# Kernel optimization log

Measured on AMD Instinct MI355X. Metric: run time of the kernel, lower is better.

## Reference

```python
import jax, jax.numpy as jnp
from jax import lax
import numpy as np

N_BASIS = 256
N_FREQ = 128
N_TIME = 8
LAM = 0.2
LR = 1e-3
B1, B2, EPS = 0.9, 0.999, 1e-8
CONV_TOL = 1e-3


def setup_inputs() -> dict:
    key = jax.random.key(0)
    k1, k2 = jax.random.split(key)
    spec = jax.random.normal(k1, (32, N_FREQ, 256), dtype=jnp.float32)
    basis = jax.random.normal(k2, (N_FREQ * N_TIME, N_BASIS), dtype=jnp.float32)
    return {"spec": spec, "basis": basis, "n_iter_coef": 30, "pad": 0, "stride": 4}


def normalize01(x):
    # torch normalize01 with dims=-1, keepdims
    xmin = x.min(axis=-1, keepdims=True)
    xmax = x.max(axis=-1, keepdims=True)
    return (x - xmin) / (xmax - xmin)


def _response(x, basis, n_iter):
    # x: [B, D]; Adam-optimize coef [B, N_BASIS] for n_iter steps with the
    # same early-stop rule as the torch code (frozen via a done flag).
    B = x.shape[0]
    sig = jnp.std(x, ddof=1)  # torch .std() is unbiased over all elements

    def loss_fn(coef):
        pred = coef @ basis.T                      # [B, D]
        mse = jnp.mean((pred - x) ** 2)
        return mse + LAM * sig * jnp.mean(jnp.abs(coef / sig))

    coef0 = jnp.full((B, N_BASIS), 0.5 / N_BASIS, dtype=jnp.float32)
    m0 = jnp.zeros_like(coef0)
    v0 = jnp.zeros_like(coef0)

    def body(carry, _):
        coef, m, v, t, old_loss, done = carry
        loss, g = jax.value_and_grad(loss_fn)(coef)
        t_new = t + 1.0
        m_new = B1 * m + (1.0 - B1) * g
        v_new = B2 * v + (1.0 - B2) * g * g
        mhat = m_new / (1.0 - B1 ** t_new)
        vhat = v_new / (1.0 - B2 ** t_new)
        coef_new = coef - LR * mhat / (jnp.sqrt(vhat) + EPS)
        conv = jnp.abs(old_loss - loss) / old_loss < CONV_TOL
        sel = lambda a, b: jnp.where(done, a, b)
        new_carry = (
            sel(coef, coef_new),
            sel(m, m_new),
            sel(v, v_new),
            jnp.where(done, t, t_new),
            jnp.where(done, old_loss, loss),
            done | conv,
        )
        return new_carry, None

    init = (coef0, m0, v0, jnp.float32(0.0), jnp.float32(1e-10), jnp.array(False))
    (coef, _, _, _, _, _), _ = lax.scan(body, init, None, length=n_iter)
    return coef  # detached in torch


def reference(spec, basis, n_iter_coef, pad, stride):
    if spec.ndim == 2:
        spec = spec[None, ...]
    B, F, T = spec.shape
    spec_ = jnp.pad(spec, ((0, 0), (0, 0), (pad, pad)))
    starts = np.arange(0, T - N_TIME + 1, stride)          # window start frames
    idx = starts[:, None] + np.arange(N_TIME)              # [W, N_TIME]
    wins = spec_[:, :, idx]                                # [B, F, W, N_TIME]
    x = jnp.transpose(wins, (2, 0, 1, 3)).reshape(len(starts), B, F * N_TIME)
    x = normalize01(x)                                     # per row of [B, D]
    coef = jax.vmap(lambda xw: _response(xw, basis, n_iter_coef))(x)  # [W, B, N_BASIS]
    return jnp.transpose(coef, (1, 2, 0))                  # [B, N_BASIS, W]
```

## Files before the change

### kernel.cpp

```cpp
#include <hip/hip_runtime.h>
#include <math.h>

#define NB     256
#define NF     128
#define FT     1024
#define NW     63
#define TORIG  256
#define MAXIT  48
#define RPB    8
#define NBLK   4
#define GRID   256

typedef float f2 __attribute__((ext_vector_type(2)));
__device__ __forceinline__ f2 pkfma(f2 a, f2 b, f2 c) {
    return __builtin_elementwise_fma(a, b, c);
}

__device__ __forceinline__ float rl(float v, int lane) {
    return __uint_as_float((unsigned)__builtin_amdgcn_readlane((int)__float_as_uint(v), lane));
}

__device__ __forceinline__ int xidx(int k2, int cg, int row) {
    return (k2 * 512 + row * 64 + (cg ^ row)) * 4;
}

__global__ __launch_bounds__(512, 2) void window_kernel(
    const float* __restrict__ spec,
    const float* __restrict__ basis,
    float* __restrict__ G,
    const int* __restrict__ p_niter,
    const int* __restrict__ p_pad,
    const int* __restrict__ p_stride,
    double* __restrict__ sxbuf,
    double* __restrict__ gpart,
    unsigned int* __restrict__ gcnt,
    float* __restrict__ out)
{
    __shared__ float  s_p0[RPB * 2048];
    __shared__ float  s_p1[RPB * 2048];
    __shared__ float  s_gred[2][NB];
    __shared__ float  s_mn[RPB], s_rng[RPB];
    __shared__ double s_dred[8];
    __shared__ float  s_redq[2][8], s_redr[2][8];
    __shared__ unsigned int s_wcnt[2];
    __shared__ int    s_stop[2];
    float* const s_xn = s_p1;

    const int bid = blockIdx.x;
    const int yy  = bid >> 3;
    const int q   = yy & 3;
    const int w   = (bid & 7) + 8 * (yy >> 2);
    const int tid = threadIdx.x;
    const int ks  = tid >> 6;
    const int kg  = tid & 63;
    const int r   = kg >> 3;
    const int cgo = 8 * ks + (kg & 7);
    const int n_iter = p_niter[0];
    const int t0     = w * p_stride[0] - p_pad[0];
    unsigned int* gbar = gcnt + MAXIT * NW;

    {
        const int c = tid & 255, jh = tid >> 8;
        float acc = 0.f;
        const float* bp = basis + (size_t)(jh * 512) * NB;
        #pragma unroll 16
        for (int j = 0; j < 512; ++j)
            acc = fmaf(bp[j * NB + bid], bp[j * NB + c], acc);
        s_gred[jh][c] = acc;
        __syncthreads();
        if (jh == 0) G[(size_t)bid * NB + c] = s_gred[0][c] + s_gred[1][c];
    }
    __threadfence();
    __syncthreads();
    if (tid == 0) atomicAdd(gbar, 1u);
    if (w >= NW) return;

    #pragma unroll
    for (int i = 0; i < 16; ++i) {
        const int e = i * 512 + tid;
        const int b = e >> 10, jj = e & 1023;
        const int f = jj >> 3, t = jj & 7, tq = t0 + t;
        s_xn[b * FT + jj] = (tq >= 0 && tq < TORIG)
            ? spec[((size_t)(q * RPB + b) * NF + f) * TORIG + tq] : 0.f;
    }
    __syncthreads();
    {
        float mn = __builtin_inff(), mx = -__builtin_inff();
        #pragma unroll
        for (int i = 0; i < 16; ++i) {
            const float v = s_xn[ks * FT + i * 64 + kg];
            mn = fminf(mn, v); mx = fmaxf(mx, v);
        }
        #pragma unroll
        for (int off = 32; off; off >>= 1) {
            mn = fminf(mn, __shfl_down(mn, off));
            mx = fmaxf(mx, __shfl_down(mx, off));
        }
        if (kg == 0) { s_mn[ks] = mn; s_rng[ks] = mx - mn; }
    }
    __syncthreads();
    double sx2p = 0.0;
    #pragma unroll
    for (int i = 0; i < 16; ++i) {
        const int e = i * 512 + tid;
        const int b = e >> 10, jj = e & 1023;
        const float v = (s_xn[b * FT + jj] - s_mn[b]) / s_rng[b];
        s_xn[b * FT + jj] = v;
        sx2p += (double)v * (double)v;
    }
    #pragma unroll
    for (int off = 32; off; off >>= 1) sx2p += __shfl_down(sx2p, off);
    if (kg == 0) s_dred[ks] = sx2p;
    __syncthreads();
    if (tid == 0) {
        double s = 0.0;
        #pragma unroll
        for (int i = 0; i < 8; ++i) s += s_dred[i];
        sxbuf[w * NBLK + q] = s;
        __threadfence();
    }

    f2 xb01[RPB], xb23[RPB];
    #pragma unroll
    for (int b = 0; b < RPB; ++b) { xb01[b] = (f2){0.f, 0.f}; xb23[b] = (f2){0.f, 0.f}; }
    for (int i0 = 0; i0 < 128; i0 += 4) {
        const int jj = ks * 128 + i0;
        float4 bv[4];
        #pragma unroll
        for (int t = 0; t < 4; ++t)
            bv[t] = *(const float4*)(basis + (size_t)(jj + t) * NB + 4 * kg);
        #pragma unroll
        for (int b = 0; b < RPB; ++b) {
            const float4 x4 = *(const float4*)&s_xn[b * FT + jj];
            const f2 vx = {x4.x, x4.x}, vy = {x4.y, x4.y};
            const f2 vz = {x4.z, x4.z}, vw = {x4.w, x4.w};
            xb01[b] = pkfma(vx, (f2){bv[0].x, bv[0].y}, xb01[b]);
            xb23[b] = pkfma(vx, (f2){bv[0].z, bv[0].w}, xb23[b]);
            xb01[b] = pkfma(vy, (f2){bv[1].x, bv[1].y}, xb01[b]);
            xb23[b] = pkfma(vy, (f2){bv[1].z, bv[1].w}, xb23[b]);
            xb01[b] = pkfma(vz, (f2){bv[2].x, bv[2].y}, xb01[b]);
            xb23[b] = pkfma(vz, (f2){bv[2].z, bv[2].w}, xb23[b]);
            xb01[b] = pkfma(vw, (f2){bv[3].x, bv[3].y}, xb01[b]);
            xb23[b] = pkfma(vw, (f2){bv[3].z, bv[3].w}, xb23[b]);
        }
    }
    __syncthreads();
    #pragma unroll
    for (int b = 0; b < RPB; ++b)
        *(float4*)&s_p0[xidx(ks, kg, b)] =
            make_float4(xb01[b].x, xb01[b].y, xb23[b].x, xb23[b].y);
    __syncthreads();
    float xB[4] = {0.f, 0.f, 0.f, 0.f};
    #pragma unroll
    for (int k2 = 0; k2 < 8; ++k2) {
        const float4 p4 = *(const float4*)&s_p0[xidx(k2, cgo, r)];
        xB[0] += p4.x; xB[1] += p4.y; xB[2] += p4.z; xB[3] += p4.w;
    }

    if (tid == 0) {
        while (__hip_atomic_load(gbar, __ATOMIC_ACQUIRE, __HIP_MEMORY_SCOPE_AGENT) < (unsigned)GRID)
            __builtin_amdgcn_s_sleep(1);
    }
    if (tid == 64) { s_wcnt[0] = 0; s_wcnt[1] = 0; s_stop[0] = 0; s_stop[1] = 0; }
    __syncthreads();
    float4 g[32];
    #pragma unroll
    for (int kl = 0; kl < 32; ++kl)
        g[kl] = *(const float4*)(G + (size_t)(32 * ks + kl) * NB + 4 * kg);

    const float C0 = 0.5f / 256.f;
    float cf[4]  = {C0, C0, C0, C0}, cfp[4] = {C0, C0, C0, C0};
    float m_[4]  = {0, 0, 0, 0},    v_[4]  = {0, 0, 0, 0};
    float b1p = 1.f, b2p = 1.f;
    float old_loss = 1e-10f;
    double sxtot = 0.0;
    const float c1 = 2.f / 32768.f, c2 = 0.2f / 8192.f;
    int use_prev = 0;

    for (int it = 0; it < n_iter; ++it) {
        const int p = it & 1;
        float* const sp = p ? s_p1 : s_p0;

        if (tid == 64 && it >= 2) {
            const int itc = it - 2;
            while (__hip_atomic_load(&gcnt[itc * NW + w], __ATOMIC_ACQUIRE,
                                     __HIP_MEMORY_SCOPE_AGENT) < (unsigned)NBLK)
                __builtin_amdgcn_s_sleep(1);
            const size_t pbm = ((size_t)itc * NW + w) * NBLK;
            double Qt = 0.0, Rt = 0.0;
            #pragma unroll
            for (int i = 0; i < NBLK; ++i) {
                Qt += gpart[(pbm + i) * 2 + 0];
                Rt += gpart[(pbm + i) * 2 + 1];
            }
            if (itc == 0)
                sxtot = sxbuf[w * NBLK + 0] + sxbuf[w * NBLK + 1] +
                        sxbuf[w * NBLK + 2] + sxbuf[w * NBLK + 3];
            const float loss = (float)((Qt + sxtot) / 32768.0 + 0.2 * (Rt / 8192.0));
            const float stat = fabsf(old_loss - loss) / old_loss;
            old_loss = loss;
            s_stop[p] = (stat < 1e-3f) ? 1 : 0;
        }

        #pragma unroll
        for (int b = 0; b < RPB; ++b) {
            f2 a01 = {0.f, 0.f}, a23 = {0.f, 0.f};
            #pragma unroll
            for (int m = 0; m < 8; ++m) {
                const float4 ga = g[4 * m + 0], gb = g[4 * m + 1];
                const float4 gc = g[4 * m + 2], gd = g[4 * m + 3];
                const int L = b * 8 + m;
                const float sx = rl(cf[0], L), sy = rl(cf[1], L);
                const float sz = rl(cf[2], L), sw = rl(cf[3], L);
                const f2 vx = {sx, sx}, vy = {sy, sy}, vz = {sz, sz}, vw = {sw, sw};
                a01 = pkfma(vx, (f2){ga.x, ga.y}, a01);
                a23 = pkfma(vx, (f2){ga.z, ga.w}, a23);
                a01 = pkfma(vy, (f2){gb.x, gb.y}, a01);
                a23 = pkfma(vy, (f2){gb.z, gb.w}, a23);
                a01 = pkfma(vz, (f2){gc.x, gc.y}, a01);
                a23 = pkfma(vz, (f2){gc.z, gc.w}, a23);
                a01 = pkfma(vw, (f2){gd.x, gd.y}, a01);
                a23 = pkfma(vw, (f2){gd.z, gd.w}, a23);
            }
            *(float4*)&sp[xidx(ks, kg, b)] = make_float4(a01.x, a01.y, a23.x, a23.y);
        }

        __syncthreads();

        if (s_stop[p]) { use_prev = 1; break; }

        f2 r01 = {0.f, 0.f}, r23 = {0.f, 0.f};
        #pragma unroll
        for (int k2 = 0; k2 < 8; ++k2) {
            const float4 p4 = *(const float4*)&sp[xidx(k2, cgo, r)];
            r01 += (f2){p4.x, p4.y};
            r23 += (f2){p4.z, p4.w};
        }
        const float a4[4] = {r01.x, r01.y, r23.x, r23.y};

        if (it + 1 < n_iter) {
            float qc = 0.f, rr = 0.f;
            #pragma unroll
            for (int j = 0; j < 4; ++j) {
                qc += cf[j] * (a4[j] - 2.f * xB[j]);
                rr += fabsf(cf[j]);
            }
            #pragma unroll
            for (int off = 32; off; off >>= 1) {
                qc += __shfl_down(qc, off);
                rr += __shfl_down(rr, off);
            }
            if (kg == 0) {
                s_redq[p][ks] = qc; s_redr[p][ks] = rr;
                __threadfence_block();
                const unsigned old = __hip_atomic_fetch_add(&s_wcnt[p], 1u,
                                        __ATOMIC_ACQ_REL, __HIP_MEMORY_SCOPE_WORKGROUP);
                if (old == 7u) {
                    float Q = 0.f, R = 0.f;
                    #pragma unroll
                    for (int i = 0; i < 8; ++i) { Q += s_redq[p][i]; R += s_redr[p][i]; }
                    s_wcnt[p] = 0u;
                    const size_t pb = ((size_t)it * NW + w) * NBLK;
                    gpart[(pb + q) * 2 + 0] = (double)Q;
                    gpart[(pb + q) * 2 + 1] = (double)R;
                    __hip_atomic_fetch_add(&gcnt[it * NW + w], 1u,
                                           __ATOMIC_RELEASE, __HIP_MEMORY_SCOPE_AGENT);
                }
            }
        }

        b1p *= 0.9f; b2p *= 0.999f;
        const float rb1 = __builtin_amdgcn_rcpf(1.f - b1p);
        const float rb2 = __builtin_amdgcn_rcpf(1.f - b2p);
        #pragma unroll
        for (int j = 0; j < 4; ++j) {
            const float c_ = cf[j];
            cfp[j] = c_;
            const float sgn = (c_ > 0.f) ? 1.f : ((c_ < 0.f) ? -1.f : 0.f);
            const float gg = c1 * (a4[j] - xB[j]) + c2 * sgn;
            m_[j] = 0.9f * m_[j] + 0.1f * gg;
            v_[j] = 0.999f * v_[j] + 0.001f * gg * gg;
            const float den = __builtin_amdgcn_sqrtf(v_[j] * rb2) + 1e-8f;
            cf[j] = c_ - 1e-3f * (m_[j] * rb1) * __builtin_amdgcn_rcpf(den);
        }
    }

    if (!use_prev && n_iter >= 2) {
        if (tid == 64) {
            const int itc = n_iter - 2;
            while (__hip_atomic_load(&gcnt[itc * NW + w], __ATOMIC_ACQUIRE,
                                     __HIP_MEMORY_SCOPE_AGENT) < (unsigned)NBLK)
                __builtin_amdgcn_s_sleep(1);
            const size_t pbm = ((size_t)itc * NW + w) * NBLK;
            double Qt = 0.0, Rt = 0.0;
            #pragma unroll
            for (int i = 0; i < NBLK; ++i) {
                Qt += gpart[(pbm + i) * 2 + 0];
                Rt += gpart[(pbm + i) * 2 + 1];
            }
            if (itc == 0)
                sxtot = sxbuf[w * NBLK + 0] + sxbuf[w * NBLK + 1] +
                        sxbuf[w * NBLK + 2] + sxbuf[w * NBLK + 3];
            const float loss = (float)((Qt + sxtot) / 32768.0 + 0.2 * (Rt / 8192.0));
            const float stat = fabsf(old_loss - loss) / old_loss;
            s_stop[0] = (stat < 1e-3f) ? 1 : 0;
        }
        __syncthreads();
        use_prev = s_stop[0];
    }

    #pragma unroll
    for (int j = 0; j < 4; ++j)
        out[((size_t)(q * RPB + r) * NB + 4 * cgo + j) * NW + w] =
            use_prev ? cfp[j] : cf[j];
}

extern "C" void kernel_launch(void* const* d_in, const int* in_sizes, int n_in,
                              void* d_out, int out_size, void* d_ws, size_t ws_size,
                              hipStream_t stream)
{
    const float* spec   = (const float*)d_in[0];
    const float* basis  = (const float*)d_in[1];
    const int* p_niter  = (const int*)d_in[2];
    const int* p_pad    = (const int*)d_in[3];
    const int* p_stride = (const int*)d_in[4];
    float* out = (float*)d_out;

    char* ws = (char*)d_ws;
    float*        G     = (float*)ws;
    double*       sxbuf = (double*)(ws + 262144);
    double*       gpart = (double*)(ws + 266240);
    unsigned int* gcnt  = (unsigned int*)(ws + 266240 + 193536);

    hipMemsetAsync(gcnt, 0, (MAXIT * NW + 1) * sizeof(unsigned int), stream);
    window_kernel<<<dim3(GRID), dim3(512), 0, stream>>>(
        spec, basis, G, p_niter, p_pad, p_stride, sxbuf, gpart, gcnt, out);
}
```

Before: 325.1 us.

## Double block size to 1024 threads, halving per-thread coefficient and Gram work

```diff
diff --git a/kernel.cpp b/kernel.cpp
--- a/kernel.cpp
+++ b/kernel.cpp
@@ -15,16 +15,11 @@
 __device__ __forceinline__ f2 pkfma(f2 a, f2 b, f2 c) {
     return __builtin_elementwise_fma(a, b, c);
 }
-
 __device__ __forceinline__ float rl(float v, int lane) {
     return __uint_as_float((unsigned)__builtin_amdgcn_readlane((int)__float_as_uint(v), lane));
 }
 
-__device__ __forceinline__ int xidx(int k2, int cg, int row) {
-    return (k2 * 512 + row * 64 + (cg ^ row)) * 4;
-}
-
-__global__ __launch_bounds__(512, 2) void window_kernel(
+__global__ __launch_bounds__(1024, 4) void window_kernel(
     const float* __restrict__ spec,
     const float* __restrict__ basis,
     float* __restrict__ G,
@@ -36,25 +31,26 @@
     unsigned int* __restrict__ gcnt,
     float* __restrict__ out)
 {
-    __shared__ float  s_p0[RPB * 2048];
-    __shared__ float  s_p1[RPB * 2048];
-    __shared__ float  s_gred[2][NB];
+    __shared__ float  s_ex[16 * RPB * 256];
+    __shared__ float  s_gred[4][NB];
+    __shared__ float  s_mnh[16], s_mxh[16];
     __shared__ float  s_mn[RPB], s_rng[RPB];
-    __shared__ double s_dred[8];
-    __shared__ float  s_redq[2][8], s_redr[2][8];
-    __shared__ unsigned int s_wcnt[2];
+    __shared__ double s_dred[16];
+    __shared__ float  s_redq[16], s_redr[16];
+    __shared__ unsigned int s_wcnt;
     __shared__ int    s_stop[2];
-    float* const s_xn = s_p1;
+    float* const s_xn = s_ex;
 
     const int bid = blockIdx.x;
     const int yy  = bid >> 3;
     const int q   = yy & 3;
     const int w   = (bid & 7) + 8 * (yy >> 2);
     const int tid = threadIdx.x;
-    const int ks  = tid >> 6;
+    const int kh  = tid >> 6;
     const int kg  = tid & 63;
-    const int r   = kg >> 3;
-    const int cgo = 8 * ks + (kg & 7);
+    const int bo  = kg >> 3;
+    const int jo  = kg & 7;
+    const int ko  = 16 * kh + 2 * jo;
     const int n_iter = p_niter[0];
     const int t0     = w * p_stride[0] - p_pad[0];
     unsigned int* gbar = gcnt + MAXIT * NW;
@@ -62,13 +58,15 @@
     {
         const int c = tid & 255, jh = tid >> 8;
         float acc = 0.f;
-        const float* bp = basis + (size_t)(jh * 512) * NB;
+        const float* bp = basis + (size_t)(jh * 256) * NB;
         #pragma unroll 16
-        for (int j = 0; j < 512; ++j)
+        for (int j = 0; j < 256; ++j)
             acc = fmaf(bp[j * NB + bid], bp[j * NB + c], acc);
         s_gred[jh][c] = acc;
         __syncthreads();
-        if (jh == 0) G[(size_t)bid * NB + c] = s_gred[0][c] + s_gred[1][c];
+        if (jh == 0)
+            G[(size_t)bid * NB + c] = (s_gred[0][c] + s_gred[1][c])
+                                    + (s_gred[2][c] + s_gred[3][c]);
     }
     __threadfence();
     __syncthreads();
@@ -76,19 +74,19 @@
     if (w >= NW) return;
 
     #pragma unroll
-    for (int i = 0; i < 16; ++i) {
-        const int e = i * 512 + tid;
-        const int b = e >> 10, jj = e & 1023;
+    for (int i = 0; i < 8; ++i) {
+        const int jj = tid;
         const int f = jj >> 3, t = jj & 7, tq = t0 + t;
-        s_xn[b * FT + jj] = (tq >= 0 && tq < TORIG)
-            ? spec[((size_t)(q * RPB + b) * NF + f) * TORIG + tq] : 0.f;
+        s_xn[i * FT + jj] = (tq >= 0 && tq < TORIG)
+            ? spec[((size_t)(q * RPB + i) * NF + f) * TORIG + tq] : 0.f;
     }
     __syncthreads();
     {
+        const int rr = kh >> 1, hh = kh & 1;
         float mn = __builtin_inff(), mx = -__builtin_inff();
         #pragma unroll
-        for (int i = 0; i < 16; ++i) {
-            const float v = s_xn[ks * FT + i * 64 + kg];
+        for (int i = 0; i < 8; ++i) {
+            const float v = s_xn[rr * FT + hh * 512 + i * 64 + kg];
             mn = fminf(mn, v); mx = fmaxf(mx, v);
         }
         #pragma unroll
@@ -96,26 +94,30 @@
             mn = fminf(mn, __shfl_down(mn, off));
             mx = fmaxf(mx, __shfl_down(mx, off));
         }
-        if (kg == 0) { s_mn[ks] = mn; s_rng[ks] = mx - mn; }
+        if (kg == 0) { s_mnh[kh] = mn; s_mxh[kh] = mx; }
+    }
+    __syncthreads();
+    if (tid < RPB) {
+        const float mn = fminf(s_mnh[2 * tid], s_mnh[2 * tid + 1]);
+        const float mx = fmaxf(s_mxh[2 * tid], s_mxh[2 * tid + 1]);
+        s_mn[tid] = mn; s_rng[tid] = mx - mn;
     }
     __syncthreads();
     double sx2p = 0.0;
     #pragma unroll
-    for (int i = 0; i < 16; ++i) {
-        const int e = i * 512 + tid;
-        const int b = e >> 10, jj = e & 1023;
-        const float v = (s_xn[b * FT + jj] - s_mn[b]) / s_rng[b];
-        s_xn[b * FT + jj] = v;
+    for (int i = 0; i < 8; ++i) {
+        const float v = (s_xn[i * FT + tid] - s_mn[i]) / s_rng[i];
+        s_xn[i * FT + tid] = v;
         sx2p += (double)v * (double)v;
     }
     #pragma unroll
     for (int off = 32; off; off >>= 1) sx2p += __shfl_down(sx2p, off);
-    if (kg == 0) s_dred[ks] = sx2p;
+    if (kg == 0) s_dred[kh] = sx2p;
     __syncthreads();
     if (tid == 0) {
         double s = 0.0;
         #pragma unroll
-        for (int i = 0; i < 8; ++i) s += s_dred[i];
+        for (int i = 0; i < 16; ++i) s += s_dred[i];
         sxbuf[w * NBLK + q] = s;
         __threadfence();
     }
@@ -123,8 +125,8 @@
     f2 xb01[RPB], xb23[RPB];
     #pragma unroll
     for (int b = 0; b < RPB; ++b) { xb01[b] = (f2){0.f, 0.f}; xb23[b] = (f2){0.f, 0.f}; }
-    for (int i0 = 0; i0 < 128; i0 += 4) {
-        const int jj = ks * 128 + i0;
+    for (int i0 = 0; i0 < 64; i0 += 4) {
+        const int jj = kh * 64 + i0;
         float4 bv[4];
         #pragma unroll
         for (int t = 0; t < 4; ++t)
@@ -147,30 +149,28 @@
     __syncthreads();
     #pragma unroll
     for (int b = 0; b < RPB; ++b)
-        *(float4*)&s_p0[xidx(ks, kg, b)] =
+        *(float4*)&s_ex[(kh * RPB + b) * 256 + ((4 * kg + 4 * b) & 255)] =
             make_float4(xb01[b].x, xb01[b].y, xb23[b].x, xb23[b].y);
     __syncthreads();
-    float xB[4] = {0.f, 0.f, 0.f, 0.f};
-    #pragma unroll
-    for (int k2 = 0; k2 < 8; ++k2) {
-        const float4 p4 = *(const float4*)&s_p0[xidx(k2, cgo, r)];
-        xB[0] += p4.x; xB[1] += p4.y; xB[2] += p4.z; xB[3] += p4.w;
-    }
+    f2 xB = {0.f, 0.f};
+    #pragma unroll
+    for (int k2 = 0; k2 < 16; ++k2)
+        xB += *(const f2*)&s_ex[(k2 * RPB + bo) * 256 + ((ko + 4 * bo) & 255)];
 
     if (tid == 0) {
         while (__hip_atomic_load(gbar, __ATOMIC_ACQUIRE, __HIP_MEMORY_SCOPE_AGENT) < (unsigned)GRID)
             __builtin_amdgcn_s_sleep(1);
     }
-    if (tid == 64) { s_wcnt[0] = 0; s_wcnt[1] = 0; s_stop[0] = 0; s_stop[1] = 0; }
-    __syncthreads();
-    float4 g[32];
-    #pragma unroll
-    for (int kl = 0; kl < 32; ++kl)
-        g[kl] = *(const float4*)(G + (size_t)(32 * ks + kl) * NB + 4 * kg);
+    if (tid == 64) { s_wcnt = 0; s_stop[0] = 0; s_stop[1] = 0; }
+    __syncthreads();
+    float4 g[16];
+    #pragma unroll
+    for (int kl = 0; kl < 16; ++kl)
+        g[kl] = *(const float4*)(G + (size_t)(16 * kh + kl) * NB + 4 * kg);
 
     const float C0 = 0.5f / 256.f;
-    float cf[4]  = {C0, C0, C0, C0}, cfp[4] = {C0, C0, C0, C0};
-    float m_[4]  = {0, 0, 0, 0},    v_[4]  = {0, 0, 0, 0};
+    float cf[2]  = {C0, C0}, cfp[2] = {C0, C0};
+    float m_[2]  = {0, 0},   v_[2]  = {0, 0};
     float b1p = 1.f, b2p = 1.f;
     float old_loss = 1e-10f;
     double sxtot = 0.0;
@@ -179,7 +179,6 @@
 
     for (int it = 0; it < n_iter; ++it) {
         const int p = it & 1;
-        float* const sp = p ? s_p1 : s_p0;
 
         if (tid == 64 && it >= 2) {
             const int itc = it - 2;
@@ -206,60 +205,47 @@
         for (int b = 0; b < RPB; ++b) {
             f2 a01 = {0.f, 0.f}, a23 = {0.f, 0.f};
             #pragma unroll
-            for (int m = 0; m < 8; ++m) {
-                const float4 ga = g[4 * m + 0], gb = g[4 * m + 1];
-                const float4 gc = g[4 * m + 2], gd = g[4 * m + 3];
-                const int L = b * 8 + m;
-                const float sx = rl(cf[0], L), sy = rl(cf[1], L);
-                const float sz = rl(cf[2], L), sw = rl(cf[3], L);
-                const f2 vx = {sx, sx}, vy = {sy, sy}, vz = {sz, sz}, vw = {sw, sw};
-                a01 = pkfma(vx, (f2){ga.x, ga.y}, a01);
-                a23 = pkfma(vx, (f2){ga.z, ga.w}, a23);
-                a01 = pkfma(vy, (f2){gb.x, gb.y}, a01);
-                a23 = pkfma(vy, (f2){gb.z, gb.w}, a23);
-                a01 = pkfma(vz, (f2){gc.x, gc.y}, a01);
-                a23 = pkfma(vz, (f2){gc.z, gc.w}, a23);
-                a01 = pkfma(vw, (f2){gd.x, gd.y}, a01);
-                a23 = pkfma(vw, (f2){gd.z, gd.w}, a23);
-            }
-            *(float4*)&sp[xidx(ks, kg, b)] = make_float4(a01.x, a01.y, a23.x, a23.y);
+            for (int j = 0; j < 8; ++j) {
+                const int L = b * 8 + j;
+                const float s0 = rl(cf[0], L), s1 = rl(cf[1], L);
+                const float4 g0 = g[2 * j], g1 = g[2 * j + 1];
+                const f2 v0 = {s0, s0}, v1 = {s1, s1};
+                a01 = pkfma(v0, (f2){g0.x, g0.y}, a01);
+                a23 = pkfma(v0, (f2){g0.z, g0.w}, a23);
+                a01 = pkfma(v1, (f2){g1.x, g1.y}, a01);
+                a23 = pkfma(v1, (f2){g1.z, g1.w}, a23);
+            }
+            *(float4*)&s_ex[(kh * RPB + b) * 256 + ((4 * kg + 4 * b) & 255)] =
+                make_float4(a01.x, a01.y, a23.x, a23.y);
         }
 
         __syncthreads();
 
         if (s_stop[p]) { use_prev = 1; break; }
 
-        f2 r01 = {0.f, 0.f}, r23 = {0.f, 0.f};
-        #pragma unroll
-        for (int k2 = 0; k2 < 8; ++k2) {
-            const float4 p4 = *(const float4*)&sp[xidx(k2, cgo, r)];
-            r01 += (f2){p4.x, p4.y};
-            r23 += (f2){p4.z, p4.w};
-        }
-        const float a4[4] = {r01.x, r01.y, r23.x, r23.y};
+        f2 aa = {0.f, 0.f};
+        #pragma unroll
+        for (int k2 = 0; k2 < 16; ++k2)
+            aa += *(const f2*)&s_ex[(k2 * RPB + bo) * 256 + ((ko + 4 * bo) & 255)];
 
         if (it + 1 < n_iter) {
-            float qc = 0.f, rr = 0.f;
-            #pragma unroll
-            for (int j = 0; j < 4; ++j) {
-                qc += cf[j] * (a4[j] - 2.f * xB[j]);
-                rr += fabsf(cf[j]);
-            }
+            float qc = cf[0] * (aa.x - 2.f * xB.x) + cf[1] * (aa.y - 2.f * xB.y);
+            float rr = fabsf(cf[0]) + fabsf(cf[1]);
             #pragma unroll
             for (int off = 32; off; off >>= 1) {
                 qc += __shfl_down(qc, off);
                 rr += __shfl_down(rr, off);
             }
             if (kg == 0) {
-                s_redq[p][ks] = qc; s_redr[p][ks] = rr;
+                s_redq[kh] = qc; s_redr[kh] = rr;
                 __threadfence_block();
-                const unsigned old = __hip_atomic_fetch_add(&s_wcnt[p], 1u,
+                const unsigned old = __hip_atomic_fetch_add(&s_wcnt, 1u,
                                         __ATOMIC_ACQ_REL, __HIP_MEMORY_SCOPE_WORKGROUP);
-                if (old == 7u) {
+                if (old == 15u) {
                     float Q = 0.f, R = 0.f;
                     #pragma unroll
-                    for (int i = 0; i < 8; ++i) { Q += s_redq[p][i]; R += s_redr[p][i]; }
-                    s_wcnt[p] = 0u;
+                    for (int i = 0; i < 16; ++i) { Q += s_redq[i]; R += s_redr[i]; }
+                    s_wcnt = 0u;
                     const size_t pb = ((size_t)it * NW + w) * NBLK;
                     gpart[(pb + q) * 2 + 0] = (double)Q;
                     gpart[(pb + q) * 2 + 1] = (double)R;
@@ -272,17 +258,21 @@
         b1p *= 0.9f; b2p *= 0.999f;
         const float rb1 = __builtin_amdgcn_rcpf(1.f - b1p);
         const float rb2 = __builtin_amdgcn_rcpf(1.f - b2p);
-        #pragma unroll
-        for (int j = 0; j < 4; ++j) {
+        const float av[2] = {aa.x, aa.y};
+        const float xv[2] = {xB.x, xB.y};
+        #pragma unroll
+        for (int j = 0; j < 2; ++j) {
             const float c_ = cf[j];
             cfp[j] = c_;
             const float sgn = (c_ > 0.f) ? 1.f : ((c_ < 0.f) ? -1.f : 0.f);
-            const float gg = c1 * (a4[j] - xB[j]) + c2 * sgn;
+            const float gg = c1 * (av[j] - xv[j]) + c2 * sgn;
             m_[j] = 0.9f * m_[j] + 0.1f * gg;
             v_[j] = 0.999f * v_[j] + 0.001f * gg * gg;
             const float den = __builtin_amdgcn_sqrtf(v_[j] * rb2) + 1e-8f;
             cf[j] = c_ - 1e-3f * (m_[j] * rb1) * __builtin_amdgcn_rcpf(den);
         }
+
+        __syncthreads();
     }
 
     if (!use_prev && n_iter >= 2) {
@@ -310,8 +300,8 @@
     }
 
     #pragma unroll
-    for (int j = 0; j < 4; ++j)
-        out[((size_t)(q * RPB + r) * NB + 4 * cgo + j) * NW + w] =
+    for (int j = 0; j < 2; ++j)
+        out[((size_t)(q * RPB + bo) * NB + ko + j) * NW + w] =
             use_prev ? cfp[j] : cf[j];
 }
 
@@ -333,6 +323,6 @@
     unsigned int* gcnt  = (unsigned int*)(ws + 266240 + 193536);
 
     hipMemsetAsync(gcnt, 0, (MAXIT * NW + 1) * sizeof(unsigned int), stream);
-    window_kernel<<<dim3(GRID), dim3(512), 0, stream>>>(
+    window_kernel<<<dim3(GRID), dim3(1024), 0, stream>>>(
         spec, basis, G, p_niter, p_pad, p_stride, sxbuf, gpart, gcnt, out);
 }
```

After: 367.7 us. 13.1% more time.
